# Kernel optimization log

Measured on AMD Instinct MI355X. Metric: run time of the kernel, lower is better.

Reference implementation:

```python
import jax, jax.numpy as jnp
import numpy as np

BATCH = 4096  # number of rows in the sparse input matrix (static for segment_sum)


def setup_inputs() -> dict:
    key = jax.random.key(0)
    k1, k2, k3, k4 = jax.random.split(key, 4)
    nnz = 262144
    in_features, out_features = 32000, 256
    row_idx = jnp.sort(jax.random.randint(k1, (nnz,), 0, BATCH, dtype=jnp.int32))
    col_idx = jax.random.randint(k2, (nnz,), 0, in_features, dtype=jnp.int32)
    vals = jax.random.uniform(k3, (nnz,), dtype=jnp.float32)
    weight = jax.random.normal(k4, (in_features, out_features), dtype=jnp.float32) / np.sqrt(out_features)
    bias = jnp.zeros((out_features,), dtype=jnp.float32)
    return {"row_idx": row_idx, "col_idx": col_idx, "vals": vals,
            "weight": weight, "bias": bias}


def reference(row_idx, col_idx, vals, weight, bias):
    # out = sparse_input @ weight + bias
    # sparse_input is COO: (row_idx, col_idx, vals), shape [BATCH, in_features]
    # gather weight rows for each nonzero, scale by value, sum per output row
    contrib = vals[:, None] * weight[col_idx]          # [nnz, out_features]
    out = jax.ops.segment_sum(contrib, row_idx, num_segments=BATCH)  # [BATCH, out]
    return out + bias
```

## Files before the change

### kernel.cpp

```cpp
#include <hip/hip_runtime.h>


constexpr int BATCH = 4096;

__global__ void build_row_ptr(const int* __restrict__ row_idx, int nnz,
                              int* __restrict__ ptr)
{
    const int i = blockIdx.x * blockDim.x + threadIdx.x;
    if (i >= nnz) return;
    const int r  = row_idx[i];
    const int rn = (i + 1 < nnz) ? row_idx[i + 1] : BATCH;
    for (int rr = r + 1; rr <= rn; ++rr) ptr[rr] = i + 1;
    if (i == 0)
        for (int rr = 0; rr <= r; ++rr) ptr[rr] = 0;
}

__global__ __launch_bounds__(256, 8) void sparse_linear_kernel(
    const int*   __restrict__ col_idx,
    const float* __restrict__ vals,
    const float* __restrict__ weight,
    const float* __restrict__ bias,
    const int*   __restrict__ ptr,
    float*       __restrict__ out)
{
    __shared__ float4 part[4][64];

    const int wave = threadIdx.x >> 6;
    const int lane = threadIdx.x & 63;
    const int r    = blockIdx.x;

    const int start = ptr[r];
    const int end   = ptr[r + 1];
    const int len   = end - start;
    const int chunk = (len + 3) >> 2;

    int k  = start + wave * chunk;
    int ke = min(k + chunk, end);

    const float4* __restrict__ W = reinterpret_cast<const float4*>(weight);

    float4 a0 = make_float4(0.f, 0.f, 0.f, 0.f);
    float4 a1 = a0, a2 = a0, a3 = a0;

    for (; k + 4 <= ke; k += 4) {
        const int   c0 = col_idx[k + 0], c1 = col_idx[k + 1];
        const int   c2 = col_idx[k + 2], c3 = col_idx[k + 3];
        const float v0 = vals[k + 0], v1 = vals[k + 1];
        const float v2 = vals[k + 2], v3 = vals[k + 3];
        const float4 w0 = W[(size_t)c0 * 64 + lane];
        const float4 w1 = W[(size_t)c1 * 64 + lane];
        const float4 w2 = W[(size_t)c2 * 64 + lane];
        const float4 w3 = W[(size_t)c3 * 64 + lane];
        a0.x = fmaf(v0, w0.x, a0.x); a0.y = fmaf(v0, w0.y, a0.y);
        a0.z = fmaf(v0, w0.z, a0.z); a0.w = fmaf(v0, w0.w, a0.w);
        a1.x = fmaf(v1, w1.x, a1.x); a1.y = fmaf(v1, w1.y, a1.y);
        a1.z = fmaf(v1, w1.z, a1.z); a1.w = fmaf(v1, w1.w, a1.w);
        a2.x = fmaf(v2, w2.x, a2.x); a2.y = fmaf(v2, w2.y, a2.y);
        a2.z = fmaf(v2, w2.z, a2.z); a2.w = fmaf(v2, w2.w, a2.w);
        a3.x = fmaf(v3, w3.x, a3.x); a3.y = fmaf(v3, w3.y, a3.y);
        a3.z = fmaf(v3, w3.z, a3.z); a3.w = fmaf(v3, w3.w, a3.w);
    }
    for (; k < ke; ++k) {
        const int   c = col_idx[k];
        const float v = vals[k];
        const float4 w = W[(size_t)c * 64 + lane];
        a0.x = fmaf(v, w.x, a0.x); a0.y = fmaf(v, w.y, a0.y);
        a0.z = fmaf(v, w.z, a0.z); a0.w = fmaf(v, w.w, a0.w);
    }

    float4 acc;
    acc.x = (a0.x + a1.x) + (a2.x + a3.x);
    acc.y = (a0.y + a1.y) + (a2.y + a3.y);
    acc.z = (a0.z + a1.z) + (a2.z + a3.z);
    acc.w = (a0.w + a1.w) + (a2.w + a3.w);

    part[wave][lane] = acc;
    __syncthreads();

    if (wave == 0) {
        const float4 p0 = part[0][lane], p1 = part[1][lane];
        const float4 p2 = part[2][lane], p3 = part[3][lane];
        const float4 b  = reinterpret_cast<const float4*>(bias)[lane];
        float4 o;
        o.x = ((p0.x + p1.x) + (p2.x + p3.x)) + b.x;
        o.y = ((p0.y + p1.y) + (p2.y + p3.y)) + b.y;
        o.z = ((p0.z + p1.z) + (p2.z + p3.z)) + b.z;
        o.w = ((p0.w + p1.w) + (p2.w + p3.w)) + b.w;
        reinterpret_cast<float4*>(out)[(size_t)r * 64 + lane] = o;
    }
}

extern "C" void kernel_launch(void* const* d_in, const int* in_sizes, int n_in,
                              void* d_out, int out_size, void* d_ws, size_t ws_size,
                              hipStream_t stream)
{
    const int*   row_idx = (const int*)  d_in[0];
    const int*   col_idx = (const int*)  d_in[1];
    const float* vals    = (const float*)d_in[2];
    const float* weight  = (const float*)d_in[3];
    const float* bias    = (const float*)d_in[4];
    float*       out     = (float*)      d_out;
    const int    nnz     = in_sizes[0];

    int* row_ptr = (int*)d_ws;

    hipLaunchKernelGGL(build_row_ptr, dim3((nnz + 255) / 256), dim3(256), 0, stream,
                       row_idx, nnz, row_ptr);
    hipLaunchKernelGGL(sparse_linear_kernel, dim3(BATCH), dim3(256), 0, stream,
                       col_idx, vals, weight, bias, row_ptr, out);
}
```

Measured before the change: 114.6 us.

## Gather bf16-converted weights and process two rows per block

A fused prep kernel builds the row pointers and also converts the fp32 weight matrix to bf16 in the workspace on every call. The main kernel then gathers 8-byte bf16 weight slices instead of 16-byte fp32 ones, which halves the bytes moved per nonzero in the bandwidth-bound gather. Each block now handles two rows with two waves per row, unrolls by 8 with wave-uniform index loads, and handles the tail with a masked unrolled loop. In exchange, every call pays a full read and write pass over the weights, and products are accumulated from bf16-rounded weights, which loses accuracy.

```diff
diff --git a/kernel.cpp b/kernel.cpp
--- a/kernel.cpp
+++ b/kernel.cpp
@@ -1,92 +1,129 @@
 #include <hip/hip_runtime.h>
+#include <hip/hip_bf16.h>
 
 
 constexpr int BATCH = 4096;
 
-__global__ void build_row_ptr(const int* __restrict__ row_idx, int nnz,
-                              int* __restrict__ ptr)
-{
-    const int i = blockIdx.x * blockDim.x + threadIdx.x;
-    if (i >= nnz) return;
-    const int r  = row_idx[i];
-    const int rn = (i + 1 < nnz) ? row_idx[i + 1] : BATCH;
-    for (int rr = r + 1; rr <= rn; ++rr) ptr[rr] = i + 1;
-    if (i == 0)
-        for (int rr = 0; rr <= r; ++rr) ptr[rr] = 0;
+__device__ inline unsigned short f2bf(float f) {
+    unsigned u = __float_as_uint(f);
+    unsigned r = (u + 0x7FFFu + ((u >> 16) & 1u)) >> 16;
+    return (unsigned short)r;
 }
 
-__global__ __launch_bounds__(256, 8) void sparse_linear_kernel(
-    const int*   __restrict__ col_idx,
-    const float* __restrict__ vals,
+__global__ __launch_bounds__(256) void prep_kernel(
     const float* __restrict__ weight,
-    const float* __restrict__ bias,
-    const int*   __restrict__ ptr,
-    float*       __restrict__ out)
+    unsigned short* __restrict__ wb,
+    const int* __restrict__ row_idx, int nnz,
+    int* __restrict__ ptr,
+    int n_w4, int conv_blocks)
+{
+    if ((int)blockIdx.x < conv_blocks) {
+        const int t = blockIdx.x * 256 + threadIdx.x;
+        if (t < n_w4) {
+            const float4 f = reinterpret_cast<const float4*>(weight)[t];
+            ushort4 o;
+            o.x = f2bf(f.x); o.y = f2bf(f.y); o.z = f2bf(f.z); o.w = f2bf(f.w);
+            reinterpret_cast<ushort4*>(wb)[t] = o;
+        }
+    } else {
+        const int i = (blockIdx.x - conv_blocks) * 256 + threadIdx.x;
+        if (i >= nnz) return;
+        const int r  = row_idx[i];
+        const int rn = (i + 1 < nnz) ? row_idx[i + 1] : BATCH;
+        for (int rr = r + 1; rr <= rn; ++rr) ptr[rr] = i + 1;
+        if (i == 0)
+            for (int rr = 0; rr <= r; ++rr) ptr[rr] = 0;
+    }
+}
+
+__device__ inline void fma_bf(float v, uint2 w, float4& acc) {
+    acc.x = fmaf(v, __uint_as_float(w.x << 16),          acc.x);
+    acc.y = fmaf(v, __uint_as_float(w.x & 0xFFFF0000u), acc.y);
+    acc.z = fmaf(v, __uint_as_float(w.y << 16),          acc.z);
+    acc.w = fmaf(v, __uint_as_float(w.y & 0xFFFF0000u), acc.w);
+}
+
+__global__ __launch_bounds__(256, 8) void sparse_linear_bf16(
+    const int*            __restrict__ col_idx,
+    const float*          __restrict__ vals,
+    const unsigned short* __restrict__ wb,
+    const float*          __restrict__ bias,
+    const int*            __restrict__ ptr,
+    float*                __restrict__ out,
+    int nnz)
 {
     __shared__ float4 part[4][64];
 
     const int wave = threadIdx.x >> 6;
     const int lane = threadIdx.x & 63;
-    const int r    = blockIdx.x;
+    const int rloc = wave >> 1;
+    const int half = wave & 1;
+    const int r    = blockIdx.x * 2 + rloc;
 
     const int start = ptr[r];
     const int end   = ptr[r + 1];
-    const int len   = end - start;
-    const int chunk = (len + 3) >> 2;
+    const int chunk = (end - start + 1) >> 1;
 
-    int k  = start + wave * chunk;
+    int k  = start + half * chunk;
     int ke = min(k + chunk, end);
 
-    const float4* __restrict__ W = reinterpret_cast<const float4*>(weight);
+    const uint2* __restrict__ W = reinterpret_cast<const uint2*>(wb);
 
-    float4 a0 = make_float4(0.f, 0.f, 0.f, 0.f);
-    float4 a1 = a0, a2 = a0, a3 = a0;
+    float4 acc = make_float4(0.f, 0.f, 0.f, 0.f);
 
-    for (; k + 4 <= ke; k += 4) {
-        const int   c0 = col_idx[k + 0], c1 = col_idx[k + 1];
-        const int   c2 = col_idx[k + 2], c3 = col_idx[k + 3];
-        const float v0 = vals[k + 0], v1 = vals[k + 1];
-        const float v2 = vals[k + 2], v3 = vals[k + 3];
-        const float4 w0 = W[(size_t)c0 * 64 + lane];
-        const float4 w1 = W[(size_t)c1 * 64 + lane];
-        const float4 w2 = W[(size_t)c2 * 64 + lane];
-        const float4 w3 = W[(size_t)c3 * 64 + lane];
-        a0.x = fmaf(v0, w0.x, a0.x); a0.y = fmaf(v0, w0.y, a0.y);
-        a0.z = fmaf(v0, w0.z, a0.z); a0.w = fmaf(v0, w0.w, a0.w);
-        a1.x = fmaf(v1, w1.x, a1.x); a1.y = fmaf(v1, w1.y, a1.y);
-        a1.z = fmaf(v1, w1.z, a1.z); a1.w = fmaf(v1, w1.w, a1.w);
-        a2.x = fmaf(v2, w2.x, a2.x); a2.y = fmaf(v2, w2.y, a2.y);
-        a2.z = fmaf(v2, w2.z, a2.z); a2.w = fmaf(v2, w2.w, a2.w);
-        a3.x = fmaf(v3, w3.x, a3.x); a3.y = fmaf(v3, w3.y, a3.y);
-        a3.z = fmaf(v3, w3.z, a3.z); a3.w = fmaf(v3, w3.w, a3.w);
-    }
-    for (; k < ke; ++k) {
-        const int   c = col_idx[k];
-        const float v = vals[k];
-        const float4 w = W[(size_t)c * 64 + lane];
-        a0.x = fmaf(v, w.x, a0.x); a0.y = fmaf(v, w.y, a0.y);
-        a0.z = fmaf(v, w.z, a0.z); a0.w = fmaf(v, w.w, a0.w);
+    while (k + 8 <= ke) {
+        const int kb = __builtin_amdgcn_readfirstlane(k);
+        const int   c0 = col_idx[kb + 0], c1 = col_idx[kb + 1];
+        const int   c2 = col_idx[kb + 2], c3 = col_idx[kb + 3];
+        const int   c4 = col_idx[kb + 4], c5 = col_idx[kb + 5];
+        const int   c6 = col_idx[kb + 6], c7 = col_idx[kb + 7];
+        const float v0 = vals[kb + 0], v1 = vals[kb + 1];
+        const float v2 = vals[kb + 2], v3 = vals[kb + 3];
+        const float v4 = vals[kb + 4], v5 = vals[kb + 5];
+        const float v6 = vals[kb + 6], v7 = vals[kb + 7];
+        const uint2 w0 = W[(size_t)c0 * 64 + lane];
+        const uint2 w1 = W[(size_t)c1 * 64 + lane];
+        const uint2 w2 = W[(size_t)c2 * 64 + lane];
+        const uint2 w3 = W[(size_t)c3 * 64 + lane];
+        const uint2 w4 = W[(size_t)c4 * 64 + lane];
+        const uint2 w5 = W[(size_t)c5 * 64 + lane];
+        const uint2 w6 = W[(size_t)c6 * 64 + lane];
+        const uint2 w7 = W[(size_t)c7 * 64 + lane];
+        fma_bf(v0, w0, acc); fma_bf(v1, w1, acc);
+        fma_bf(v2, w2, acc); fma_bf(v3, w3, acc);
+        fma_bf(v4, w4, acc); fma_bf(v5, w5, acc);
+        fma_bf(v6, w6, acc); fma_bf(v7, w7, acc);
+        k += 8;
     }
 
-    float4 acc;
-    acc.x = (a0.x + a1.x) + (a2.x + a3.x);
-    acc.y = (a0.y + a1.y) + (a2.y + a3.y);
-    acc.z = (a0.z + a1.z) + (a2.z + a3.z);
-    acc.w = (a0.w + a1.w) + (a2.w + a3.w);
+    const int rem = ke - k;
+    if (rem > 0) {
+        const int kb = __builtin_amdgcn_readfirstlane(k);
+        #pragma unroll
+        for (int j = 0; j < 8; ++j) {
+            const int   kk = min(kb + j, nnz - 1);
+            const int   c  = col_idx[kk];
+            const float v  = (j < rem) ? vals[kk] : 0.0f;
+            const uint2 w  = W[(size_t)c * 64 + lane];
+            fma_bf(v, w, acc);
+        }
+    }
 
     part[wave][lane] = acc;
     __syncthreads();
 
-    if (wave == 0) {
-        const float4 p0 = part[0][lane], p1 = part[1][lane];
-        const float4 p2 = part[2][lane], p3 = part[3][lane];
-        const float4 b  = reinterpret_cast<const float4*>(bias)[lane];
+    if (threadIdx.x < 128) {
+        const int rl = threadIdx.x >> 6;
+        const int ln = threadIdx.x & 63;
+        const float4 p0 = part[2 * rl + 0][ln];
+        const float4 p1 = part[2 * rl + 1][ln];
+        const float4 b  = reinterpret_cast<const float4*>(bias)[ln];
         float4 o;
-        o.x = ((p0.x + p1.x) + (p2.x + p3.x)) + b.x;
-        o.y = ((p0.y + p1.y) + (p2.y + p3.y)) + b.y;
-        o.z = ((p0.z + p1.z) + (p2.z + p3.z)) + b.z;
-        o.w = ((p0.w + p1.w) + (p2.w + p3.w)) + b.w;
-        reinterpret_cast<float4*>(out)[(size_t)r * 64 + lane] = o;
+        o.x = (p0.x + p1.x) + b.x;
+        o.y = (p0.y + p1.y) + b.y;
+        o.z = (p0.z + p1.z) + b.z;
+        o.w = (p0.w + p1.w) + b.w;
+        reinterpret_cast<float4*>(out)[(size_t)(blockIdx.x * 2 + rl) * 64 + ln] = o;
     }
 }
 
@@ -101,11 +138,17 @@
     const float* bias    = (const float*)d_in[4];
     float*       out     = (float*)      d_out;
     const int    nnz     = in_sizes[0];
+    const int    w_elems = in_sizes[3];
 
-    int* row_ptr = (int*)d_ws;
+    unsigned short* wb      = (unsigned short*)d_ws;
+    int*            row_ptr = (int*)((char*)d_ws + (32u << 20));
 
-    hipLaunchKernelGGL(build_row_ptr, dim3((nnz + 255) / 256), dim3(256), 0, stream,
-                       row_idx, nnz, row_ptr);
-    hipLaunchKernelGGL(sparse_linear_kernel, dim3(BATCH), dim3(256), 0, stream,
-                       col_idx, vals, weight, bias, row_ptr, out);
+    const int n_w4        = w_elems / 4;
+    const int conv_blocks = (n_w4 + 255) / 256;
+    const int rptr_blocks = (nnz + 255) / 256;
+
+    hipLaunchKernelGGL(prep_kernel, dim3(conv_blocks + rptr_blocks), dim3(256), 0, stream,
+                       weight, wb, row_idx, nnz, row_ptr, n_w4, conv_blocks);
+    hipLaunchKernelGGL(sparse_linear_bf16, dim3(BATCH / 2), dim3(256), 0, stream,
+                       col_idx, vals, wb, bias, row_ptr, out, nnz);
 }
```

New measurement: 105.1 us. 1.09x faster.
